# Performance work log

Measured on AMD Instinct MI355X. Metric: run time of the kernel, lower is better.

The kernel has to match this reference:

```python
import jax, jax.numpy as jnp
import numpy as np
from jax.ops import segment_sum

N_NODES = 50000
N_EDGES = 800000

def setup_inputs() -> dict:
    key = jax.random.key(0)
    ks = jax.random.split(key, 8)
    def glorot(k, shape):
        fan_in, fan_out = shape
        lim = jnp.sqrt(6.0 / (fan_in + fan_out))
        return jax.random.uniform(k, shape, jnp.float32, -lim, lim)
    return {
        'features': jax.random.normal(ks[0], (N_NODES, 1433), jnp.float32),
        'edge_index': jax.random.randint(ks[1], (2, N_EDGES), 0, N_NODES, jnp.int64),
        'W1': glorot(ks[2], (1433, 256)), 'b1': jnp.zeros((256,), jnp.float32),
        'W2': glorot(ks[3], (256, 32)),  'b2': jnp.zeros((32,), jnp.float32),
        'W3': glorot(ks[4], (32, 7)),    'b3': jnp.zeros((7,), jnp.float32),
    }

def _graph_conv(x, W, b, src, dst, c_src, c_dst, n):
    # DGL GraphConv, norm='both', in_feats > out_feats: weight first, then SpMM.
    h = (x * c_src[:, None]) @ W          # [N, out]
    agg = segment_sum(h[src], dst, num_segments=n)  # sparse neighbor sum
    return agg * c_dst[:, None] + b

def reference(features, edge_index, W1, b1, W2, b2, W3, b3):
    n = features.shape[0]
    src, dst = edge_index[0], edge_index[1]
    ones = jnp.ones((src.shape[0],), jnp.float32)
    deg_out = jnp.maximum(segment_sum(ones, src, num_segments=n), 1.0)
    deg_in = jnp.maximum(segment_sum(ones, dst, num_segments=n), 1.0)
    c_src = jax.lax.rsqrt(deg_out)
    c_dst = jax.lax.rsqrt(deg_in)
    x1 = jax.nn.relu(_graph_conv(features, W1, b1, src, dst, c_src, c_dst, n))
    x2 = jax.nn.relu(_graph_conv(x1, W2, b2, src, dst, c_src, c_dst, n))
    x3 = _graph_conv(x2, W3, b3, src, dst, c_src, c_dst, n)
    return jax.nn.log_softmax(x3, axis=1)
```

## Files before the change

### kernel.cpp

```cpp
#include <hip/hip_runtime.h>
#include <math.h>

typedef unsigned short u16;
typedef unsigned int u32;
typedef __attribute__((ext_vector_type(8))) short bf16x8;
typedef __attribute__((ext_vector_type(4))) float f32x4;

#define NN 50000
#define NE 800000
#define F0 1433
#define KP 1440
#define MP 50048
#define D1 256
#define D2 32
#define NB 196
#define HB 3125
#define PB 2048
#define SB 3125

__device__ __forceinline__ float bf2f(u16 h) { return __uint_as_float(((u32)h) << 16); }
__device__ __forceinline__ u16 f2bf(float f) {
  u32 u = __float_as_uint(f);
  u32 r = (u + 0x7FFFu + ((u >> 16) & 1u)) >> 16;
  return (u16)r;
}
__device__ __forceinline__ u32 pack2(float lo, float hi) {
  return (u32)f2bf(lo) | ((u32)f2bf(hi) << 16);
}

__device__ __forceinline__ void gl16(const void* g, void* l) {
  __builtin_amdgcn_global_load_lds((const __attribute__((address_space(1))) u32*)g,
                                   (__attribute__((address_space(3))) u32*)l, 16, 0, 0);
}

__global__ __launch_bounds__(256) void k_histpad(const int* __restrict__ ei,
                                                 int* __restrict__ cs, int* __restrict__ cd,
                                                 const float* __restrict__ F, u16* __restrict__ P) {
  if (blockIdx.x < HB) {
    const int e = blockIdx.x * 256 + threadIdx.x;
    if (e < NE) {
      atomicAdd(&cs[ei[e]], 1);
      atomicAdd(&cd[ei[NE + e]], 1);
    }
    return;
  }
  const int tid0 = (blockIdx.x - HB) * 256 + threadIdx.x;
  const int NCH = MP * (KP / 8);
  for (int c = tid0; c < NCH; c += PB * 256) {
    const int i = c / (KP / 8);
    const int k = (c - i * (KP / 8)) * 8;
    uint4 v = {0u, 0u, 0u, 0u};
    if (i < NN) {
      const float* fr = F + (size_t)i * F0 + k;
      float f[8];
#pragma unroll
      for (int j = 0; j < 8; ++j) f[j] = (k + j < F0) ? fr[j] : 0.f;
      v.x = pack2(f[0], f[1]);
      v.y = pack2(f[2], f[3]);
      v.z = pack2(f[4], f[5]);
      v.w = pack2(f[6], f[7]);
    }
    *(uint4*)(P + (size_t)i * KP + k) = v;
  }
}

__global__ __launch_bounds__(256) void k_scan1(const int* __restrict__ cd, int* __restrict__ bsum) {
  __shared__ int sh[256];
  const int t = threadIdx.x;
  const int i = blockIdx.x * 256 + t;
  sh[t] = (i < NN) ? cd[i] : 0;
  __syncthreads();
  for (int o = 128; o > 0; o >>= 1) {
    if (t < o) sh[t] += sh[t + o];
    __syncthreads();
  }
  if (t == 0) bsum[blockIdx.x] = sh[0];
}

__global__ __launch_bounds__(256) void k_scan2(const int* __restrict__ bsum, int* __restrict__ boff) {
  __shared__ int sh[256];
  const int t = threadIdx.x;
  const int v = (t < NB) ? bsum[t] : 0;
  sh[t] = v;
  __syncthreads();
  for (int o = 1; o < 256; o <<= 1) {
    int x = (t >= o) ? sh[t - o] : 0;
    __syncthreads();
    sh[t] += x;
    __syncthreads();
  }
  if (t < NB) boff[t] = sh[t] - v;
}

__global__ __launch_bounds__(256) void k_scan3(const int* __restrict__ cd, const int* __restrict__ cs,
                                               const int* __restrict__ boff,
                                               int* __restrict__ row, int* __restrict__ cur,
                                               float* __restrict__ cdst, float* __restrict__ csrc) {
  __shared__ int sh[256];
  const int t = threadIdx.x;
  const int i = blockIdx.x * 256 + t;
  const int v = (i < NN) ? cd[i] : 0;
  sh[t] = v;
  __syncthreads();
  for (int o = 1; o < 256; o <<= 1) {
    int x = (t >= o) ? sh[t - o] : 0;
    __syncthreads();
    sh[t] += x;
    __syncthreads();
  }
  if (i < NN) {
    const int start = boff[blockIdx.x] + sh[t] - v;
    row[i] = start;
    cur[i] = start;
    if (i == NN - 1) row[NN] = start + v;
    cdst[i] = rsqrtf(fmaxf((float)v, 1.0f));
    csrc[i] = rsqrtf(fmaxf((float)cs[i], 1.0f));
  }
}

__global__ __launch_bounds__(256) void k_scatprep(const int* __restrict__ ei,
                                                  int* __restrict__ cur, int* __restrict__ csr,
                                                  const float* __restrict__ W1, const float* __restrict__ W2,
                                                  u16* __restrict__ W1T, u16* __restrict__ W2T) {
  const int bid = blockIdx.x;
  const int t = threadIdx.x;
  if (bid < SB) {
    const int e = bid * 256 + t;
    if (e < NE) {
      const int d = ei[NE + e];
      const int p = atomicAdd(&cur[d], 1);
      csr[p] = ei[e];
    }
    return;
  }
  const int b = bid - SB;
  if (b < KP) {
    W1T[(size_t)t * KP + b] = (b < F0) ? f2bf(W1[(size_t)b * D1 + t]) : (u16)0;
  } else {
    const int idx = (b - KP) * 256 + t;
    const int k = idx & 255, n = idx >> 8;
    W2T[n * 256 + k] = f2bf(W2[k * 32 + n]);
  }
}

__global__ __launch_bounds__(256) void k_gemm1(const u16* __restrict__ A, const u16* __restrict__ BT,
                                               const float* __restrict__ csrc, u16* __restrict__ H) {
  __shared__ u16 As[128 * 32];
  __shared__ u16 Bs[128 * 32];
  const int tid = threadIdx.x;
  const int wave = tid >> 6, lane = tid & 63;
  const int l16 = lane & 15, quad = lane >> 4;
  const int waveM = wave & 1, waveN = wave >> 1;

  const int wg = blockIdx.x;
  const int xcd = wg & 7, idx = wg >> 3;
  const int swz = (xcd < 6) ? xcd * 98 + idx : 588 + (xcd - 6) * 97 + idx;
  const int tn = swz & 1, tm = swz >> 1;

  f32x4 acc[4][4];
#pragma unroll
  for (int mi = 0; mi < 4; ++mi)
#pragma unroll
    for (int ni = 0; ni < 4; ++ni) acc[mi][ni] = f32x4{0.f, 0.f, 0.f, 0.f};

  const int c0 = wave * 64 + lane;
  const int rA0 = c0 >> 2, qA0 = (c0 & 3) * 8;
  const u16* Ab = A + (size_t)tm * 128 * KP;
  const u16* Bb = BT + (size_t)tn * 128 * KP;
  u16* As0 = As + (wave * 64) * 8;
  u16* As1 = As + (wave * 64 + 256) * 8;
  u16* Bs0 = Bs + (wave * 64) * 8;
  u16* Bs1 = Bs + (wave * 64 + 256) * 8;
  const size_t off0 = (size_t)rA0 * KP + qA0;
  const size_t off1 = (size_t)(rA0 + 64) * KP + qA0;

  for (int kt = 0; kt < KP / 32; ++kt) {
    const int k0 = kt * 32;
    __syncthreads();
    gl16(Ab + off0 + k0, As0);
    gl16(Ab + off1 + k0, As1);
    gl16(Bb + off0 + k0, Bs0);
    gl16(Bb + off1 + k0, Bs1);
    __syncthreads();
    bf16x8 af[4], bfr[4];
#pragma unroll
    for (int mi = 0; mi < 4; ++mi)
      af[mi] = *(const bf16x8*)(As + ((waveM * 64 + mi * 16 + l16) * 32 + quad * 8));
#pragma unroll
    for (int ni = 0; ni < 4; ++ni)
      bfr[ni] = *(const bf16x8*)(Bs + ((waveN * 64 + ni * 16 + l16) * 32 + quad * 8));
#pragma unroll
    for (int mi = 0; mi < 4; ++mi)
#pragma unroll
      for (int ni = 0; ni < 4; ++ni)
        acc[mi][ni] = __builtin_amdgcn_mfma_f32_16x16x32_bf16(af[mi], bfr[ni], acc[mi][ni], 0, 0, 0);
  }

  const int rbase = tm * 128 + waveM * 64 + quad * 4;
  const int cbase = tn * 128 + waveN * 64 + l16;
#pragma unroll
  for (int mi = 0; mi < 4; ++mi) {
#pragma unroll
    for (int e = 0; e < 4; ++e) {
      const int i = rbase + mi * 16 + e;
      if (i < NN) {
        const float cs = csrc[i];
#pragma unroll
        for (int ni = 0; ni < 4; ++ni)
          H[(size_t)i * D1 + cbase + ni * 16] = f2bf(acc[mi][ni][e] * cs);
      }
    }
  }
}

__global__ __launch_bounds__(256) void k_spmm1f(const int* __restrict__ row, const int* __restrict__ csr,
                                                const u16* __restrict__ h1, const float* __restrict__ cdst,
                                                const float* __restrict__ csrc, const float* __restrict__ b1,
                                                u16* __restrict__ x) {
  const int d = blockIdx.x * 4 + (threadIdx.x >> 6);
  const int lane = threadIdx.x & 63;
  const int rs = row[d], re = row[d + 1];
  float a0 = 0.f, a1 = 0.f, a2 = 0.f, a3 = 0.f;
  int e = rs;
  for (; e + 3 < re; e += 4) {
    const int s0 = csr[e], s1 = csr[e + 1], s2 = csr[e + 2], s3 = csr[e + 3];
    const ushort4 v0 = *(const ushort4*)(h1 + (size_t)s0 * D1 + lane * 4);
    const ushort4 v1 = *(const ushort4*)(h1 + (size_t)s1 * D1 + lane * 4);
    const ushort4 v2 = *(const ushort4*)(h1 + (size_t)s2 * D1 + lane * 4);
    const ushort4 v3 = *(const ushort4*)(h1 + (size_t)s3 * D1 + lane * 4);
    a0 += (bf2f(v0.x) + bf2f(v1.x)) + (bf2f(v2.x) + bf2f(v3.x));
    a1 += (bf2f(v0.y) + bf2f(v1.y)) + (bf2f(v2.y) + bf2f(v3.y));
    a2 += (bf2f(v0.z) + bf2f(v1.z)) + (bf2f(v2.z) + bf2f(v3.z));
    a3 += (bf2f(v0.w) + bf2f(v1.w)) + (bf2f(v2.w) + bf2f(v3.w));
  }
  for (; e < re; ++e) {
    const int s0 = csr[e];
    const ushort4 v0 = *(const ushort4*)(h1 + (size_t)s0 * D1 + lane * 4);
    a0 += bf2f(v0.x); a1 += bf2f(v0.y); a2 += bf2f(v0.z); a3 += bf2f(v0.w);
  }
  const float cd = cdst[d], cs = csrc[d];
  const float4 bb = *(const float4*)(b1 + lane * 4);
  const float r0 = fmaxf(a0 * cd + bb.x, 0.f) * cs;
  const float r1 = fmaxf(a1 * cd + bb.y, 0.f) * cs;
  const float r2 = fmaxf(a2 * cd + bb.z, 0.f) * cs;
  const float r3 = fmaxf(a3 * cd + bb.w, 0.f) * cs;
  ushort4 o;
  o.x = f2bf(r0); o.y = f2bf(r1); o.z = f2bf(r2); o.w = f2bf(r3);
  *(ushort4*)(x + (size_t)d * D1 + lane * 4) = o;
}

__global__ __launch_bounds__(256) void k_gemm2(const u16* __restrict__ A, const u16* __restrict__ BT,
                                               u16* __restrict__ H) {
  __shared__ u16 As[128 * 32];
  __shared__ u16 Bs[32 * 32];
  const int tid = threadIdx.x;
  const int wave = tid >> 6, lane = tid & 63;
  const int l16 = lane & 15, quad = lane >> 4;
  const int tm = blockIdx.x;

  f32x4 acc[2][2];
#pragma unroll
  for (int mi = 0; mi < 2; ++mi)
#pragma unroll
    for (int ni = 0; ni < 2; ++ni) acc[mi][ni] = f32x4{0.f, 0.f, 0.f, 0.f};

  const int r0 = tid >> 2, q0 = (tid & 3) * 8;
  int rowA0 = tm * 128 + r0;      if (rowA0 >= NN) rowA0 = NN - 1;
  int rowA1 = tm * 128 + r0 + 64; if (rowA1 >= NN) rowA1 = NN - 1;
  for (int kt = 0; kt < 8; ++kt) {
    const int k0 = kt * 32;
    __syncthreads();
    uint4 v0 = *(const uint4*)(A + (size_t)rowA0 * D1 + k0 + q0);
    uint4 v1 = *(const uint4*)(A + (size_t)rowA1 * D1 + k0 + q0);
    *(uint4*)(As + r0 * 32 + q0) = v0;
    *(uint4*)(As + (r0 + 64) * 32 + q0) = v1;
    if (tid < 128) {
      uint4 vb = *(const uint4*)(BT + (size_t)r0 * D1 + k0 + q0);
      *(uint4*)(Bs + r0 * 32 + q0) = vb;
    }
    __syncthreads();
    bf16x8 af[2], bfr[2];
#pragma unroll
    for (int mi = 0; mi < 2; ++mi)
      af[mi] = *(const bf16x8*)(As + ((wave * 32 + mi * 16 + l16) * 32 + quad * 8));
#pragma unroll
    for (int ni = 0; ni < 2; ++ni)
      bfr[ni] = *(const bf16x8*)(Bs + ((ni * 16 + l16) * 32 + quad * 8));
#pragma unroll
    for (int mi = 0; mi < 2; ++mi)
#pragma unroll
      for (int ni = 0; ni < 2; ++ni)
        acc[mi][ni] = __builtin_amdgcn_mfma_f32_16x16x32_bf16(af[mi], bfr[ni], acc[mi][ni], 0, 0, 0);
  }

  const int rbase = tm * 128 + wave * 32 + quad * 4;
#pragma unroll
  for (int mi = 0; mi < 2; ++mi)
#pragma unroll
    for (int e = 0; e < 4; ++e) {
      const int i = rbase + mi * 16 + e;
      if (i < NN) {
#pragma unroll
        for (int ni = 0; ni < 2; ++ni)
          H[(size_t)i * D2 + ni * 16 + l16] = f2bf(acc[mi][ni][e]);
      }
    }
}

__global__ __launch_bounds__(256) void k_spmm2f(const int* __restrict__ row, const int* __restrict__ csr,
                                                const u16* __restrict__ h2, const float* __restrict__ cdst,
                                                const float* __restrict__ csrc, const float* __restrict__ b2,
                                                u16* __restrict__ x) {
  const int t = threadIdx.x;
  const int d = blockIdx.x * 8 + (t >> 5);
  const int f = t & 31;
  const int rs = row[d], re = row[d + 1];
  float acc = 0.f;
  int e = rs;
  for (; e + 3 < re; e += 4) {
    const int s0 = csr[e], s1 = csr[e + 1], s2 = csr[e + 2], s3 = csr[e + 3];
    acc += (bf2f(h2[(size_t)s0 * D2 + f]) + bf2f(h2[(size_t)s1 * D2 + f])) +
           (bf2f(h2[(size_t)s2 * D2 + f]) + bf2f(h2[(size_t)s3 * D2 + f]));
  }
  for (; e < re; ++e) acc += bf2f(h2[(size_t)csr[e] * D2 + f]);
  const float v = acc * cdst[d] + b2[f];
  x[(size_t)d * D2 + f] = f2bf(fmaxf(v, 0.f) * csrc[d]);
}

__global__ __launch_bounds__(256) void k_l3(const u16* __restrict__ x, const float* __restrict__ W3,
                                            float* __restrict__ h3) {
  __shared__ float w3s[224];
  const int t = threadIdx.x;
  if (t < 224) w3s[t] = W3[t];
  __syncthreads();
  const int i = blockIdx.x * 256 + t;
  if (i >= NN) return;
  const uint4* p = (const uint4*)(x + (size_t)i * D2);
  union { uint4 v[4]; u16 s[32]; } u;
  u.v[0] = p[0]; u.v[1] = p[1]; u.v[2] = p[2]; u.v[3] = p[3];
  float acc[7];
#pragma unroll
  for (int c = 0; c < 7; ++c) acc[c] = 0.f;
#pragma unroll
  for (int k = 0; k < 32; ++k) {
    const float xv = bf2f(u.s[k]);
#pragma unroll
    for (int c = 0; c < 7; ++c) acc[c] += xv * w3s[k * 7 + c];
  }
  float* o = h3 + (size_t)i * 8;
#pragma unroll
  for (int c = 0; c < 7; ++c) o[c] = acc[c];
}

__global__ __launch_bounds__(256) void k_spmm3f(const int* __restrict__ row, const int* __restrict__ csr,
                                                const float* __restrict__ h3, const float* __restrict__ cdst,
                                                const float* __restrict__ b3, float* __restrict__ out) {
  const int t = threadIdx.x;
  const int d = blockIdx.x * 32 + (t >> 3);
  const int c = t & 7;
  if (d >= NN) return;
  const int rs = row[d], re = row[d + 1];
  float acc = 0.f;
  if (c < 7) {
    int e = rs;
    for (; e + 1 < re; e += 2)
      acc += h3[(size_t)csr[e] * 8 + c] + h3[(size_t)csr[e + 1] * 8 + c];
    if (e < re) acc += h3[(size_t)csr[e] * 8 + c];
  }
  const float v = (c < 7) ? (acc * cdst[d] + b3[c]) : -INFINITY;
  float m = v;
  m = fmaxf(m, __shfl_xor(m, 1));
  m = fmaxf(m, __shfl_xor(m, 2));
  m = fmaxf(m, __shfl_xor(m, 4));
  float s = (c < 7) ? expf(v - m) : 0.f;
  s += __shfl_xor(s, 1);
  s += __shfl_xor(s, 2);
  s += __shfl_xor(s, 4);
  const float l = logf(s);
  if (c < 7) out[(size_t)d * 7 + c] = v - m - l;
}

static const size_t O_CSRC = 0;
static const size_t O_CDST = 200192;
static const size_t O_ROW  = 400384;
static const size_t O_CUR  = 601088;
static const size_t O_CNTS = 801792;
static const size_t O_CNTD = 1002496;
static const size_t O_BSUM = 1203200;
static const size_t O_BOFF = 1204224;
static const size_t O_CSR  = 1205248;
static const size_t O_W1T  = 4405248;
static const size_t O_W2T  = 5142528;
static const size_t O_H1   = 5158912;
static const size_t O_PADA = 30758912;
static const size_t O_X1S  = O_PADA;
static const size_t O_H2   = O_PADA + 25600000;
static const size_t O_X2S  = O_PADA + 28800000;
static const size_t O_H3   = O_PADA + 32000000;

extern "C" void kernel_launch(void* const* d_in, const int* in_sizes, int n_in,
                              void* d_out, int out_size, void* d_ws, size_t ws_size,
                              hipStream_t stream) {
  const float* feat = (const float*)d_in[0];
  const int* ei     = (const int*)d_in[1];
  const float* W1   = (const float*)d_in[2];
  const float* b1   = (const float*)d_in[3];
  const float* W2   = (const float*)d_in[4];
  const float* b2   = (const float*)d_in[5];
  const float* W3   = (const float*)d_in[6];
  const float* b3   = (const float*)d_in[7];
  float* out = (float*)d_out;

  char* ws = (char*)d_ws;
  float* c_src = (float*)(ws + O_CSRC);
  float* c_dst = (float*)(ws + O_CDST);
  int* row  = (int*)(ws + O_ROW);
  int* cur  = (int*)(ws + O_CUR);
  int* cnts = (int*)(ws + O_CNTS);
  int* cntd = (int*)(ws + O_CNTD);
  int* bsum = (int*)(ws + O_BSUM);
  int* boff = (int*)(ws + O_BOFF);
  int* csr  = (int*)(ws + O_CSR);
  u16* W1T  = (u16*)(ws + O_W1T);
  u16* W2T  = (u16*)(ws + O_W2T);
  u16* h1   = (u16*)(ws + O_H1);
  u16* padA = (u16*)(ws + O_PADA);
  u16* x1s  = (u16*)(ws + O_X1S);
  u16* h2   = (u16*)(ws + O_H2);
  u16* x2s  = (u16*)(ws + O_X2S);
  float* h3 = (float*)(ws + O_H3);

  hipMemsetAsync(cnts, 0, (size_t)NN * 4, stream);
  hipMemsetAsync(cntd, 0, (size_t)NN * 4, stream);
  k_histpad<<<HB + PB, 256, 0, stream>>>(ei, cnts, cntd, feat, padA);
  k_scan1<<<NB, 256, 0, stream>>>(cntd, bsum);
  k_scan2<<<1, 256, 0, stream>>>(bsum, boff);
  k_scan3<<<NB, 256, 0, stream>>>(cntd, cnts, boff, row, cur, c_dst, c_src);
  k_scatprep<<<SB + KP + 32, 256, 0, stream>>>(ei, cur, csr, W1, W2, W1T, W2T);

  k_gemm1<<<782, 256, 0, stream>>>(padA, W1T, c_src, h1);
  k_spmm1f<<<NN / 4, 256, 0, stream>>>(row, csr, h1, c_dst, c_src, b1, x1s);

  k_gemm2<<<MP / 128, 256, 0, stream>>>(x1s, W2T, h2);
  k_spmm2f<<<NN / 8, 256, 0, stream>>>(row, csr, h2, c_dst, c_src, b2, x2s);

  k_l3<<<(NN + 255) / 256, 256, 0, stream>>>(x2s, W3, h3);
  k_spmm3f<<<(NN + 31) / 32, 256, 0, stream>>>(row, csr, h3, c_dst, b3, out);
}
```

Baseline: 769.3 us.

## Fuse fp32-to-bf16 feature conversion into GEMM1 A-tile loading

Drops the separate pass that converts the 50000x1433 fp32 feature matrix into a padded bf16 buffer. GEMM1 now reads fp32 features directly with register prefetch one k-tile ahead, converts them with packed bf16 conversion instructions, and writes them to LDS. This removes a large write and re-read of the padded intermediate. The cost is unaligned fp32 loads, redundant reads for out-of-range rows, special-case handling of the tail column, and loss of async global-to-LDS loads for A.

After: 710.3 us. -7.7%, faster.

```diff
diff --git a/kernel.cpp b/kernel.cpp
--- a/kernel.cpp
+++ b/kernel.cpp
@@ -5,6 +5,7 @@
 typedef unsigned int u32;
 typedef __attribute__((ext_vector_type(8))) short bf16x8;
 typedef __attribute__((ext_vector_type(4))) float f32x4;
+typedef float f32x4u __attribute__((vector_size(16), aligned(4)));
 
 #define NN 50000
 #define NE 800000
@@ -15,7 +16,6 @@
 #define D2 32
 #define NB 196
 #define HB 3125
-#define PB 2048
 #define SB 3125
 
 __device__ __forceinline__ float bf2f(u16 h) { return __uint_as_float(((u32)h) << 16); }
@@ -24,8 +24,10 @@
   u32 r = (u + 0x7FFFu + ((u >> 16) & 1u)) >> 16;
   return (u16)r;
 }
-__device__ __forceinline__ u32 pack2(float lo, float hi) {
-  return (u32)f2bf(lo) | ((u32)f2bf(hi) << 16);
+__device__ __forceinline__ u32 cvtpk(float lo, float hi) {
+  u32 r;
+  asm("v_cvt_pk_bf16_f32 %0, %1, %2" : "=v"(r) : "v"(lo), "v"(hi));
+  return r;
 }
 
 __device__ __forceinline__ void gl16(const void* g, void* l) {
@@ -33,34 +35,12 @@
                                    (__attribute__((address_space(3))) u32*)l, 16, 0, 0);
 }
 
-__global__ __launch_bounds__(256) void k_histpad(const int* __restrict__ ei,
-                                                 int* __restrict__ cs, int* __restrict__ cd,
-                                                 const float* __restrict__ F, u16* __restrict__ P) {
-  if (blockIdx.x < HB) {
-    const int e = blockIdx.x * 256 + threadIdx.x;
-    if (e < NE) {
-      atomicAdd(&cs[ei[e]], 1);
-      atomicAdd(&cd[ei[NE + e]], 1);
-    }
-    return;
-  }
-  const int tid0 = (blockIdx.x - HB) * 256 + threadIdx.x;
-  const int NCH = MP * (KP / 8);
-  for (int c = tid0; c < NCH; c += PB * 256) {
-    const int i = c / (KP / 8);
-    const int k = (c - i * (KP / 8)) * 8;
-    uint4 v = {0u, 0u, 0u, 0u};
-    if (i < NN) {
-      const float* fr = F + (size_t)i * F0 + k;
-      float f[8];
-#pragma unroll
-      for (int j = 0; j < 8; ++j) f[j] = (k + j < F0) ? fr[j] : 0.f;
-      v.x = pack2(f[0], f[1]);
-      v.y = pack2(f[2], f[3]);
-      v.z = pack2(f[4], f[5]);
-      v.w = pack2(f[6], f[7]);
-    }
-    *(uint4*)(P + (size_t)i * KP + k) = v;
+__global__ __launch_bounds__(256) void k_hist(const int* __restrict__ ei,
+                                              int* __restrict__ cs, int* __restrict__ cd) {
+  const int e = blockIdx.x * 256 + threadIdx.x;
+  if (e < NE) {
+    atomicAdd(&cs[ei[e]], 1);
+    atomicAdd(&cd[ei[NE + e]], 1);
   }
 }
 
@@ -143,7 +123,8 @@
   }
 }
 
-__global__ __launch_bounds__(256) void k_gemm1(const u16* __restrict__ A, const u16* __restrict__ BT,
+__global__ __launch_bounds__(256) void k_gemm1(const float* __restrict__ F,
+                                               const u16* __restrict__ BT,
                                                const float* __restrict__ csrc, u16* __restrict__ H) {
   __shared__ u16 As[128 * 32];
   __shared__ u16 Bs[128 * 32];
@@ -165,23 +146,56 @@
 
   const int c0 = wave * 64 + lane;
   const int rA0 = c0 >> 2, qA0 = (c0 & 3) * 8;
-  const u16* Ab = A + (size_t)tm * 128 * KP;
+  int ga0 = tm * 128 + rA0;        if (ga0 >= NN) ga0 = NN - 1;
+  int ga1 = tm * 128 + rA0 + 64;   if (ga1 >= NN) ga1 = NN - 1;
+  const float* a0p = F + (size_t)ga0 * F0 + qA0;
+  const float* a1p = F + (size_t)ga1 * F0 + qA0;
+  const bool fix0 = (ga0 == NN - 1) && (qA0 == 24);
+  const bool fix1 = (ga1 == NN - 1) && (qA0 == 24);
+
   const u16* Bb = BT + (size_t)tn * 128 * KP;
-  u16* As0 = As + (wave * 64) * 8;
-  u16* As1 = As + (wave * 64 + 256) * 8;
   u16* Bs0 = Bs + (wave * 64) * 8;
   u16* Bs1 = Bs + (wave * 64 + 256) * 8;
-  const size_t off0 = (size_t)rA0 * KP + qA0;
-  const size_t off1 = (size_t)(rA0 + 64) * KP + qA0;
+  const size_t offB0 = (size_t)rA0 * KP + qA0;
+  const size_t offB1 = (size_t)(rA0 + 64) * KP + qA0;
+  uint4* As0w = (uint4*)As + c0;
+  uint4* As1w = (uint4*)As + (c0 + 256);
+
+  f32x4u va0 = *(const f32x4u*)(a0p);
+  f32x4u vb0 = *(const f32x4u*)(a0p + 4);
+  f32x4u va1 = *(const f32x4u*)(a1p);
+  f32x4u vb1 = *(const f32x4u*)(a1p + 4);
 
   for (int kt = 0; kt < KP / 32; ++kt) {
     const int k0 = kt * 32;
     __syncthreads();
-    gl16(Ab + off0 + k0, As0);
-    gl16(Ab + off1 + k0, As1);
-    gl16(Bb + off0 + k0, Bs0);
-    gl16(Bb + off1 + k0, Bs1);
-    __syncthreads();
+    uint4 w0, w1;
+    w0.x = cvtpk(va0[0], va0[1]); w0.y = cvtpk(va0[2], va0[3]);
+    w0.z = cvtpk(vb0[0], vb0[1]); w0.w = cvtpk(vb0[2], vb0[3]);
+    w1.x = cvtpk(va1[0], va1[1]); w1.y = cvtpk(va1[2], va1[3]);
+    w1.z = cvtpk(vb1[0], vb1[1]); w1.w = cvtpk(vb1[2], vb1[3]);
+    *As0w = w0;
+    *As1w = w1;
+    gl16(Bb + offB0 + k0, Bs0);
+    gl16(Bb + offB1 + k0, Bs1);
+    __syncthreads();
+    if (kt < 44) {
+      const int kn = k0 + 32;
+      va0 = *(const f32x4u*)(a0p + kn); vb0 = *(const f32x4u*)(a0p + kn + 4);
+      va1 = *(const f32x4u*)(a1p + kn); vb1 = *(const f32x4u*)(a1p + kn + 4);
+      if (kt == 43) {
+        if (fix0) {
+          float lastv = F[(size_t)(NN - 1) * F0 + 1432];
+          va0[0] = lastv; va0[1] = 0.f; va0[2] = 0.f; va0[3] = 0.f;
+          vb0[0] = 0.f;   vb0[1] = 0.f; vb0[2] = 0.f; vb0[3] = 0.f;
+        }
+        if (fix1) {
+          float lastv = F[(size_t)(NN - 1) * F0 + 1432];
+          va1[0] = lastv; va1[1] = 0.f; va1[2] = 0.f; va1[3] = 0.f;
+          vb1[0] = 0.f;   vb1[1] = 0.f; vb1[2] = 0.f; vb1[3] = 0.f;
+        }
+      }
+    }
     bf16x8 af[4], bfr[4];
 #pragma unroll
     for (int mi = 0; mi < 4; ++mi)
@@ -392,11 +406,10 @@
 static const size_t O_W1T  = 4405248;
 static const size_t O_W2T  = 5142528;
 static const size_t O_H1   = 5158912;
-static const size_t O_PADA = 30758912;
-static const size_t O_X1S  = O_PADA;
-static const size_t O_H2   = O_PADA + 25600000;
-static const size_t O_X2S  = O_PADA + 28800000;
-static const size_t O_H3   = O_PADA + 32000000;
+static const size_t O_X1S  = 30758912;
+static const size_t O_H2   = O_X1S + 25600000;
+static const size_t O_X2S  = O_X1S + 28800000;
+static const size_t O_H3   = O_X1S + 32000000;
 
 extern "C" void kernel_launch(void* const* d_in, const int* in_sizes, int n_in,
                               void* d_out, int out_size, void* d_ws, size_t ws_size,
@@ -424,7 +437,6 @@
   u16* W1T  = (u16*)(ws + O_W1T);
   u16* W2T  = (u16*)(ws + O_W2T);
   u16* h1   = (u16*)(ws + O_H1);
-  u16* padA = (u16*)(ws + O_PADA);
   u16* x1s  = (u16*)(ws + O_X1S);
   u16* h2   = (u16*)(ws + O_H2);
   u16* x2s  = (u16*)(ws + O_X2S);
@@ -432,13 +444,13 @@
 
   hipMemsetAsync(cnts, 0, (size_t)NN * 4, stream);
   hipMemsetAsync(cntd, 0, (size_t)NN * 4, stream);
-  k_histpad<<<HB + PB, 256, 0, stream>>>(ei, cnts, cntd, feat, padA);
+  k_hist<<<HB, 256, 0, stream>>>(ei, cnts, cntd);
   k_scan1<<<NB, 256, 0, stream>>>(cntd, bsum);
   k_scan2<<<1, 256, 0, stream>>>(bsum, boff);
   k_scan3<<<NB, 256, 0, stream>>>(cntd, cnts, boff, row, cur, c_dst, c_src);
   k_scatprep<<<SB + KP + 32, 256, 0, stream>>>(ei, cur, csr, W1, W2, W1T, W2T);
 
-  k_gemm1<<<782, 256, 0, stream>>>(padA, W1T, c_src, h1);
+  k_gemm1<<<782, 256, 0, stream>>>(feat, W1T, c_src, h1);
   k_spmm1f<<<NN / 4, 256, 0, stream>>>(row, csr, h1, c_dst, c_src, b1, x1s);
 
   k_gemm2<<<MP / 128, 256, 0, stream>>>(x1s, W2T, h2);
```
